# Performance work log

Hardware: AMD Instinct MI355X
Metric: run time of the kernel (lower is better)

Reference implementation:

```python
import jax, jax.numpy as jnp
import numpy as np

N = 50000   # drug nodes
R = 8       # relations (= n_classes)
E = 200000  # edges per relation
ED = 400000 # decoder edges


def _deg_norm(idx, n):
    deg = jax.ops.segment_sum(jnp.ones(idx.shape, jnp.float32), idx, num_segments=n)
    return jnp.where(deg > 0, jax.lax.rsqrt(jnp.maximum(deg, 1.0)), 0.0)


def hetero_conv(x, src, dst, W, b, n):
    # DGL HeteroGraphConv(sum) of GraphConv(norm='both') per relation, single node type.
    out = jnp.zeros((n, W.shape[2]), x.dtype)
    for r in range(W.shape[0]):
        s, d = src[r], dst[r]
        ns = _deg_norm(s, n)  # out-degree^{-1/2} (src norm)
        nd = _deg_norm(d, n)  # in-degree^{-1/2} (dst norm)
        m = (x * ns[:, None]) @ W[r]                       # [n, dout]
        agg = jax.ops.segment_sum(m[s], d, num_segments=n)  # gather+scatter [E, dout]
        out = out + agg * nd[:, None] + b[r]
    return out


def hgcn_layer(x, src, dst, Wa, ba, Wb, bb, n):
    h = hetero_conv(x, src, dst, Wa, ba, n)
    h = jax.nn.relu(h)
    return hetero_conv(h, src, dst, Wb, bb, n)


def setup_inputs() -> dict:
    key = jax.random.key(0)
    ks = jax.random.split(key, 16)
    s = 0.02
    return {
        "node2_features": jax.random.normal(ks[0], (N, 256), jnp.float32),
        "mpnn_features": jax.random.normal(ks[1], (N, 300), jnp.float32),
        "src": jax.random.randint(ks[2], (R, E), 0, N, jnp.int32),
        "dst": jax.random.randint(ks[3], (R, E), 0, N, jnp.int32),
        "dec_src": jax.random.randint(ks[4], (ED,), 0, N, jnp.int32),
        "dec_dst": jax.random.randint(ks[5], (ED,), 0, N, jnp.int32),
        "W2a": jax.random.normal(ks[6], (R, 256, 256), jnp.float32) * s,
        "b2a": jnp.zeros((R, 256), jnp.float32),
        "W2b": jax.random.normal(ks[7], (R, 256, 128), jnp.float32) * s,
        "b2b": jnp.zeros((R, 128), jnp.float32),
        "W3a": jax.random.normal(ks[8], (R, 300, 256), jnp.float32) * s,
        "b3a": jnp.zeros((R, 256), jnp.float32),
        "W3b": jax.random.normal(ks[9], (R, 256, 128), jnp.float32) * s,
        "b3b": jnp.zeros((R, 128), jnp.float32),
        "Wp1": jax.random.normal(ks[10], (512, 256), jnp.float32) * s,
        "bp1": jnp.zeros((256,), jnp.float32),
        "Wp2": jax.random.normal(ks[11], (256, R), jnp.float32) * s,
        "bp2": jnp.zeros((R,), jnp.float32),
    }


def reference(node2_features, mpnn_features, src, dst, dec_src, dec_dst,
              W2a, b2a, W2b, b2b, W3a, b3a, W3b, b3b, Wp1, bp1, Wp2, bp2):
    h2 = hgcn_layer(node2_features, src, dst, W2a, b2a, W2b, b2b, N)  # [N, 128]
    h3 = hgcn_layer(mpnn_features, src, dst, W3a, b3a, W3b, b3b, N)   # [N, 128]
    feat = jnp.concatenate([h2, h3], axis=1)                            # [N, 256]
    # edge-wise gather-concat-MLP (note: original has NO relu between W1 and W2)
    x = jnp.concatenate([feat[dec_src], feat[dec_dst]], axis=1)          # [ED, 512]
    score = (x @ Wp1 + bp1) @ Wp2 + bp2                                  # [ED, R]
    return score
```

## Files before the change

### kernel.cpp

```cpp
#include <hip/hip_runtime.h>
#include <hip/hip_bf16.h>

#define NN 50000
#define RR 8
#define EE 200000
#define EDD 400000
#define SCB 196
#define CH 5000
#define CHK 16

typedef __attribute__((ext_vector_type(8))) short short8;
typedef __attribute__((ext_vector_type(4))) float floatx4;

static __device__ __forceinline__ unsigned short f2bf(float f) {
    union { float f; unsigned u; } v; v.f = f;
    unsigned r = v.u + 0x7fff + ((v.u >> 16) & 1);
    return (unsigned short)(r >> 16);
}
static __device__ __forceinline__ float bf2f(unsigned short h) {
    union { unsigned u; float f; } v; v.u = ((unsigned)h) << 16;
    return v.f;
}
static __device__ __forceinline__ void gload_lds16(const unsigned short* g, unsigned short* l) {
    __builtin_amdgcn_global_load_lds(
        (const __attribute__((address_space(1))) void*)g,
        (__attribute__((address_space(3))) void*)l,
        16, 0, 0);
}

__global__ __launch_bounds__(256) void k_histp(const int* __restrict__ src, const int* __restrict__ dst,
                                               unsigned char* __restrict__ tmp) {
    __shared__ unsigned lh[12512];
    int chunk = blockIdx.x, r = blockIdx.y, which = blockIdx.z;
    const int* idx = (which ? dst : src) + (size_t)r * EE;
    for (int i = threadIdx.x; i < 12512; i += 256) lh[i] = 0;
    __syncthreads();
    int e0 = chunk * (EE / CHK);
    for (int e = e0 + threadIdx.x; e < e0 + EE / CHK; e += 256) {
        int n = idx[e];
        atomicAdd(&lh[n >> 2], 1u << ((n & 3) * 8));
    }
    __syncthreads();
    unsigned* t = (unsigned*)(tmp + (((size_t)(which * RR + r) * CHK + chunk) * 50048));
    for (int i = threadIdx.x; i < 12512; i += 256) t[i] = lh[i];
}

__global__ void k_reduce(const unsigned char* __restrict__ tmp,
                         int* __restrict__ outdeg, int* __restrict__ indeg) {
    int i = blockIdx.x * 256 + threadIdx.x;
    if (i >= 2 * RR * 12512) return;
    int wr = i / 12512;
    int wd = i - wr * 12512;
    unsigned s0 = 0, s1 = 0, s2 = 0, s3 = 0;
    const unsigned* base = (const unsigned*)(tmp + (size_t)wr * CHK * 50048) + wd;
    #pragma unroll
    for (int c = 0; c < CHK; c++) {
        unsigned v = base[(size_t)c * 12512];
        s0 += v & 255u; s1 += (v >> 8) & 255u; s2 += (v >> 16) & 255u; s3 += (v >> 24) & 255u;
    }
    int which = wr / RR, r = wr - which * RR;
    int n = wd * 4;
    int* deg = (which ? indeg : outdeg) + (size_t)r * NN;
    if (n < NN) {
        deg[n] = (int)s0;
        if (n + 1 < NN) deg[n + 1] = (int)s1;
        if (n + 2 < NN) deg[n + 2] = (int)s2;
        if (n + 3 < NN) deg[n + 3] = (int)s3;
    }
}

__global__ void k_norms(int* __restrict__ outdeg, int* __restrict__ indeg) {
    int i = blockIdx.x * blockDim.x + threadIdx.x;
    if (i >= RR * NN) return;
    int od = outdeg[i];
    int id = indeg[i];
    ((float*)outdeg)[i] = od > 0 ? rsqrtf((float)od) : 0.f;
    ((float*)indeg)[i]  = id > 0 ? rsqrtf((float)id) : 0.f;
}

__global__ void k_scanA(const int* __restrict__ indeg, int* __restrict__ bsum) {
    int r = blockIdx.y;
    int i = blockIdx.x * 256 + threadIdx.x;
    int v = (i < NN) ? indeg[(size_t)r * NN + i] : 0;
    #pragma unroll
    for (int d = 32; d > 0; d >>= 1) v += __shfl_down(v, d, 64);
    __shared__ int ws4[4];
    if ((threadIdx.x & 63) == 0) ws4[threadIdx.x >> 6] = v;
    __syncthreads();
    if (threadIdx.x == 0) bsum[r * SCB + blockIdx.x] = ws4[0] + ws4[1] + ws4[2] + ws4[3];
}

__global__ void k_scanB(int* __restrict__ bsum, int* __restrict__ offs) {
    int r = blockIdx.x;
    int t = threadIdx.x;
    int v = (t < SCB) ? bsum[r * SCB + t] : 0;
    int lane = t & 63, wid = t >> 6;
    int sv = v;
    #pragma unroll
    for (int d = 1; d < 64; d <<= 1) {
        int u = __shfl_up(sv, d, 64);
        if (lane >= d) sv += u;
    }
    __shared__ int wsum[4];
    if (lane == 63) wsum[wid] = sv;
    __syncthreads();
    int add = 0;
    for (int x = 0; x < wid; x++) add += wsum[x];
    int incl = sv + add;
    if (t < SCB) bsum[r * SCB + t] = incl - v;
    if (t == 255) offs[(size_t)r * (NN + 1) + NN] = incl;
}

__global__ void k_scanC(const int* __restrict__ indeg, const int* __restrict__ bsum,
                        int* __restrict__ offs) {
    int r = blockIdx.y;
    int i = blockIdx.x * 256 + threadIdx.x;
    int v = (i < NN) ? indeg[(size_t)r * NN + i] : 0;
    int lane = threadIdx.x & 63, wid = threadIdx.x >> 6;
    int sv = v;
    #pragma unroll
    for (int d = 1; d < 64; d <<= 1) {
        int u = __shfl_up(sv, d, 64);
        if (lane >= d) sv += u;
    }
    __shared__ int wsum[4];
    if (lane == 63) wsum[wid] = sv;
    __syncthreads();
    int add = bsum[r * SCB + blockIdx.x];
    for (int x = 0; x < wid; x++) add += wsum[x];
    if (i < NN) offs[(size_t)r * (NN + 1) + i] = sv - v + add;
}

__global__ void k_fillw(const int* __restrict__ src, const int* __restrict__ dst,
                        const int* __restrict__ offs, const float* __restrict__ ns,
                        int* __restrict__ cursor, int2* __restrict__ csrw) {
    int i = blockIdx.x * blockDim.x + threadIdx.x;
    if (i >= RR * EE) return;
    int r = i / EE;
    int s = src[i], d = dst[i];
    int pos = offs[r * (NN + 1) + d] + atomicAdd(&cursor[r * NN + d], 1);
    int2 v;
    v.x = s;
    v.y = __float_as_int(ns[(size_t)r * NN + s]);
    csrw[(size_t)r * EE + pos] = v;
}

__global__ void k_prep(const float* __restrict__ Wp1, const float* __restrict__ Wp2,
                       const float* __restrict__ bp1, const float* __restrict__ bp2,
                       const float* __restrict__ b2a, const float* __restrict__ b2b,
                       const float* __restrict__ b3a, const float* __restrict__ b3b,
                       float* __restrict__ Mcat, float* __restrict__ cvec,
                       float* __restrict__ bs) {
    int bx = blockIdx.x;
    if (bx < 16) {
        int t = bx * 256 + threadIdx.x;
        int i = t >> 4, j = t & 15;
        int half = j >> 3, jj = j & 7;
        const float* wrow = Wp1 + (size_t)(half * 256 + i) * 256;
        float s = 0.f;
        for (int k = 0; k < 256; k++) s += wrow[k] * Wp2[k * 8 + jj];
        Mcat[i * 16 + j] = s;
    } else if (bx == 16) {
        int j = threadIdx.x;
        if (j < 8) {
            float s = bp2[j];
            for (int k = 0; k < 256; k++) s += bp1[k] * Wp2[k * 8 + j];
            cvec[j] = s;
        }
    } else {
        int j = threadIdx.x;
        float s = 0.f;
        for (int r = 0; r < RR; r++) s += b2a[r * 256 + j];
        bs[j] = s;
        if (j < 128) {
            s = 0.f;
            for (int r = 0; r < RR; r++) s += b2b[r * 128 + j];
            bs[256 + j] = s;
        }
        s = 0.f;
        for (int r = 0; r < RR; r++) s += b3a[r * 256 + j];
        bs[512 + j] = s;
        if (j < 128) {
            s = 0.f;
            for (int r = 0; r < RR; r++) s += b3b[r * 128 + j];
            bs[768 + j] = s;
        }
    }
}

__global__ void k_fold(const float* __restrict__ W2b, const float* __restrict__ W3b,
                       const float* __restrict__ Mcat, const float* __restrict__ bs,
                       unsigned short* __restrict__ FmatT, float* __restrict__ cfold) {
    int bx = blockIdx.x;
    if (bx < 256) {
        int idx = bx * 256 + threadIdx.x;
        int rj = idx >> 9, i = idx & 511;
        int r = rj >> 4, j = rj & 15;
        float s = 0.f;
        if (i < 256) {
            const float* wr = W2b + ((size_t)r * 256 + i) * 128;
            for (int c = 0; c < 128; c++) s += wr[c] * Mcat[c * 16 + j];
        } else {
            const float* wr = W3b + ((size_t)r * 256 + (i - 256)) * 128;
            for (int c = 0; c < 128; c++) s += wr[c] * Mcat[(128 + c) * 16 + j];
        }
        FmatT[(size_t)rj * 512 + i] = f2bf(s);
    } else {
        int j = threadIdx.x;
        if (j < 16) {
            float s = 0.f;
            for (int c = 0; c < 128; c++)
                s += bs[256 + c] * Mcat[c * 16 + j] + bs[768 + c] * Mcat[(128 + c) * 16 + j];
            cfold[j] = s;
        }
    }
}

__global__ void k_castx(const float* __restrict__ x2, const float* __restrict__ x3,
                        unsigned short* __restrict__ XH) {
    int i = blockIdx.x * 256 + threadIdx.x;
    if (i >= NN * 560) return;
    int row = i / 560, col = i - row * 560;
    float v;
    if (col < 256) v = x2[(size_t)row * 256 + col];
    else if (col < 556) v = x3[(size_t)row * 300 + (col - 256)];
    else v = 0.f;
    XH[i] = f2bf(v);
}

__global__ void k_wt2(const float* __restrict__ W2a, const float* __restrict__ W3a,
                      unsigned short* __restrict__ WT2, unsigned short* __restrict__ WT3) {
    const float* W; unsigned short* WT; int K0, Kpad;
    if (blockIdx.y == 0) { W = W2a; WT = WT2; K0 = 256; Kpad = 256; }
    else                 { W = W3a; WT = WT3; K0 = 300; Kpad = 304; }
    int i = blockIdx.x * 256 + threadIdx.x;
    int total = 256 * RR * Kpad;
    if (i >= total) return;
    int n = i / (RR * Kpad);
    int rem = i - n * (RR * Kpad);
    int r = rem / Kpad;
    int k = rem - r * Kpad;
    float v = (k < K0) ? W[((size_t)r * K0 + k) * 256 + n] : 0.f;
    WT[i] = f2bf(v);
}

__global__ __launch_bounds__(256) void k_aggp(
        const unsigned short* __restrict__ xb,
        const int2* __restrict__ csrw, const int* __restrict__ offs,
        const float* __restrict__ nd, int nbase,
        unsigned short* __restrict__ Y2, unsigned short* __restrict__ Y3) {
    int lane = threadIdx.x & 63;
    int sub = threadIdx.x >> 6;
    int h = lane >> 5;
    int l = lane & 31;
    int bn = blockIdx.x * 4 + sub;
    int n = nbase + bn;
    int r = blockIdx.y;
    int o0 = offs[r * (NN + 1) + n];
    int o1 = offs[r * (NN + 1) + n + 1];
    o0 = __builtin_amdgcn_readfirstlane(o0);
    o1 = __builtin_amdgcn_readfirstlane(o1);
    int cnt = o1 - o0;
    float ndv = nd[(size_t)r * NN + n];
    const int2* cs = csrw + (size_t)r * EE + o0;
    bool tl = l < 6;
    float va[8], vb[8], vc[8];
    #pragma unroll
    for (int q = 0; q < 8; q++) { va[q] = 0.f; vb[q] = 0.f; vc[q] = 0.f; }

    for (int eb = 0; eb < cnt; eb += 64) {
        int rem = cnt - eb;
        int2 rec = cs[eb + min(lane, rem - 1)];
        int kmax = rem < 64 ? rem : 64;
        for (int kb = 0; kb < kmax; kb += 8) {
            #pragma unroll
            for (int u = 0; u < 4; u++) {
                int k = kb + 2 * u + h;
                int kk = k < kmax - 1 ? k : kmax - 1;
                int sidx = __shfl(rec.x, kk, 64);
                float f = __int_as_float(__shfl(rec.y, kk, 64));
                if (k >= kmax) f = 0.f;
                const unsigned short* p = xb + (size_t)(unsigned)sidx * 560;
                short8 A = *(const short8*)(p + l * 8);
                short8 B = *(const short8*)(p + 256 + l * 8);
                #pragma unroll
                for (int q = 0; q < 8; q++) {
                    va[q] += f * bf2f((unsigned short)A[q]);
                    vb[q] += f * bf2f((unsigned short)B[q]);
                }
                if (tl) {
                    short8 C = *(const short8*)(p + 512 + l * 8);
                    #pragma unroll
                    for (int q = 0; q < 8; q++) vc[q] += f * bf2f((unsigned short)C[q]);
                }
            }
        }
    }
    #pragma unroll
    for (int q = 0; q < 8; q++) {
        va[q] += __shfl_xor(va[q], 32, 64);
        vb[q] += __shfl_xor(vb[q], 32, 64);
        vc[q] += __shfl_xor(vc[q], 32, 64);
    }
    if (h == 0) {
        short8 o2, o3;
        #pragma unroll
        for (int q = 0; q < 8; q++) {
            o2[q] = (short)f2bf(va[q] * ndv);
            o3[q] = (short)f2bf(vb[q] * ndv);
        }
        *(short8*)(Y2 + (size_t)bn * 2048 + r * 256 + l * 8) = o2;
        *(short8*)(Y3 + (size_t)bn * 2432 + r * 304 + l * 8) = o3;
        if (tl) {
            short8 oc;
            #pragma unroll
            for (int q = 0; q < 8; q++) oc[q] = (short)f2bf(vc[q] * ndv);
            *(short8*)(Y3 + (size_t)bn * 2432 + r * 304 + 256 + l * 8) = oc;
        }
    }
}

template<int TN>
__global__ __launch_bounds__(256) void k_gemm_bf(
        const unsigned short* __restrict__ A, int lda,
        const unsigned short* __restrict__ BT, int ldb,
        const float* __restrict__ bias,
        const float* __restrict__ Cin, int ldcin,
        void* __restrict__ Cout, int ldc,
        int M, int K, int flags) {
    constexpr int BN = TN * 32;
    __shared__ unsigned short As[128 * 64];
    __shared__ unsigned short Bs[BN * 64];
    int m0 = blockIdx.x * 128;
    int n0 = blockIdx.y * BN;
    int t = threadIdx.x;
    int w = t >> 6, l = t & 63;
    int qm = (w >> 1) * 64, qn = (w & 1) * (TN * 16);
    int lr = l & 15, lg = l >> 4;
    int lrow = l >> 3;
    int lch  = (l & 7) ^ lrow;

    floatx4 acc[4][TN];
    #pragma unroll
    for (int a = 0; a < 4; a++)
        #pragma unroll
        for (int b = 0; b < TN; b++)
            acc[a][b] = (floatx4){0.f, 0.f, 0.f, 0.f};

    for (int k0 = 0; k0 < K; k0 += 64) {
        #pragma unroll
        for (int j = 0; j < 4; j++) {
            int seg = w * 4 + j;
            int gr = m0 + seg * 8 + lrow; if (gr > M - 1) gr = M - 1;
            gload_lds16(A + (size_t)gr * lda + k0 + lch * 8, &As[seg * 512]);
        }
        #pragma unroll
        for (int j = 0; j < TN; j++) {
            int seg = w * TN + j;
            int row = n0 + seg * 8 + lrow;
            gload_lds16(BT + (size_t)row * ldb + k0 + lch * 8, &Bs[seg * 512]);
        }
        __syncthreads();
        #pragma unroll
        for (int ks = 0; ks < 2; ks++) {
            int slot = ((ks * 4 + lg) ^ (lr & 7)) * 8;
            short8 af[4], bf[TN];
            #pragma unroll
            for (int i = 0; i < 4; i++)
                af[i] = *(const short8*)&As[(qm + i * 16 + lr) * 64 + slot];
            #pragma unroll
            for (int i = 0; i < TN; i++)
                bf[i] = *(const short8*)&Bs[(qn + i * 16 + lr) * 64 + slot];
            #pragma unroll
            for (int tm = 0; tm < 4; tm++)
                #pragma unroll
                for (int tn = 0; tn < TN; tn++)
                    acc[tm][tn] = __builtin_amdgcn_mfma_f32_16x16x32_bf16(
                        af[tm], bf[tn], acc[tm][tn], 0, 0, 0);
        }
        __syncthreads();
    }

    int addbias = flags & 1, accum = flags & 2, relu = flags & 4, outbf = flags & 8;
    #pragma unroll
    for (int tm = 0; tm < 4; tm++) {
        int rbase = m0 + qm + tm * 16 + lg * 4;
        #pragma unroll
        for (int reg = 0; reg < 4; reg++) {
            int row = rbase + reg;
            if (row >= M) continue;
            #pragma unroll
            for (int tn = 0; tn < TN; tn++) {
                int col = n0 + qn + tn * 16 + lr;
                float v = acc[tm][tn][reg];
                if (addbias) v += bias[col];
                if (accum) v += Cin[(size_t)row * ldcin + col];
                if (relu) v = fmaxf(v, 0.f);
                if (outbf) ((unsigned short*)Cout)[(size_t)row * ldc + col] = f2bf(v);
                else       ((float*)Cout)[(size_t)row * ldc + col] = v;
            }
        }
    }
}

__global__ __launch_bounds__(256) void k_gemm2(
        const unsigned short* __restrict__ Y2, const unsigned short* __restrict__ Y3,
        const unsigned short* __restrict__ WT2, const unsigned short* __restrict__ WT3,
        const float* __restrict__ bs, unsigned short* __restrict__ hb,
        int nbase, int M) {
    __shared__ unsigned short As[64 * 64];
    __shared__ unsigned short Bs[64 * 64];
    int z = blockIdx.z;
    const unsigned short* A  = z ? Y3 : Y2;
    const unsigned short* BT = z ? WT3 : WT2;
    int lda = z ? 2432 : 2048;
    int K = lda;
    const float* bias = bs + z * 512;
    int m0 = blockIdx.x * 64;
    int n0 = blockIdx.y * 64;
    int t = threadIdx.x;
    int w = t >> 6, l = t & 63;
    int qm = (w >> 1) * 32, qn = (w & 1) * 32;
    int lr = l & 15, lg = l >> 4;
    int lrow = l >> 3;
    int lch  = (l & 7) ^ lrow;

    floatx4 acc[2][2];
    #pragma unroll
    for (int a = 0; a < 2; a++)
        #pragma unroll
        for (int b = 0; b < 2; b++)
            acc[a][b] = (floatx4){0.f, 0.f, 0.f, 0.f};

    for (int k0 = 0; k0 < K; k0 += 64) {
        #pragma unroll
        for (int j = 0; j < 2; j++) {
            int seg = w * 2 + j;
            int gr = m0 + seg * 8 + lrow; if (gr > M - 1) gr = M - 1;
            gload_lds16(A + (size_t)gr * lda + k0 + lch * 8, &As[seg * 512]);
        }
        #pragma unroll
        for (int j = 0; j < 2; j++) {
            int seg = w * 2 + j;
            int row = n0 + seg * 8 + lrow;
            gload_lds16(BT + (size_t)row * lda + k0 + lch * 8, &Bs[seg * 512]);
        }
        __syncthreads();
        #pragma unroll
        for (int ks = 0; ks < 2; ks++) {
            int slot = ((ks * 4 + lg) ^ (lr & 7)) * 8;
            short8 af[2], bf[2];
            #pragma unroll
            for (int i = 0; i < 2; i++)
                af[i] = *(const short8*)&As[(qm + i * 16 + lr) * 64 + slot];
            #pragma unroll
            for (int i = 0; i < 2; i++)
                bf[i] = *(const short8*)&Bs[(qn + i * 16 + lr) * 64 + slot];
            #pragma unroll
            for (int tm = 0; tm < 2; tm++)
                #pragma unroll
                for (int tn = 0; tn < 2; tn++)
                    acc[tm][tn] = __builtin_amdgcn_mfma_f32_16x16x32_bf16(
                        af[tm], bf[tn], acc[tm][tn], 0, 0, 0);
        }
        __syncthreads();
    }

    #pragma unroll
    for (int tm = 0; tm < 2; tm++) {
        int rbase = m0 + qm + tm * 16 + lg * 4;
        #pragma unroll
        for (int reg = 0; reg < 4; reg++) {
            int row = rbase + reg;
            if (row >= M) continue;
            #pragma unroll
            for (int tn = 0; tn < 2; tn++) {
                int col = n0 + qn + tn * 16 + lr;
                float v = fmaxf(acc[tm][tn][reg] + bias[col], 0.f);
                hb[(size_t)(nbase + row) * 512 + z * 256 + col] = f2bf(v);
            }
        }
    }
}

__global__ __launch_bounds__(256) void k_aggAB(
        const int2* __restrict__ csrw, const int* __restrict__ offs,
        const float* __restrict__ nd, const float* __restrict__ G,
        const float* __restrict__ cfold, const float* __restrict__ cvec,
        float* __restrict__ AB) {
    int lane = threadIdx.x & 63, sub = threadIdx.x >> 6;
    int n = blockIdx.x * 4 + sub;
    int slot = lane >> 4, j = lane & 15;
    int jb = slot << 4;
    float acc = 0.f;
    for (int hh = 0; hh < 2; hh++) {
        int r = slot + hh * 4;
        int o0 = offs[r * (NN + 1) + n];
        int o1 = offs[r * (NN + 1) + n + 1];
        float ndv = nd[(size_t)r * NN + n];
        const int2* cs = csrw + (size_t)r * EE + o0;
        int cnt = o1 - o0;
        float t0 = 0.f, t1 = 0.f;
        for (int eb = 0; eb < cnt; eb += 16) {
            int rem = cnt - eb;
            int2 rec = cs[eb + min(j, rem - 1)];
            int kmax = rem < 16 ? rem : 16;
            for (int k = 0; k < kmax; k += 2) {
                int s0 = __shfl(rec.x, jb + k, 64);
                float f0 = __int_as_float(__shfl(rec.y, jb + k, 64));
                int k1 = k + 1 < kmax ? k + 1 : kmax - 1;
                int s1 = __shfl(rec.x, jb + k1, 64);
                float f1 = (k + 1 < kmax) ? __int_as_float(__shfl(rec.y, jb + k1, 64)) : 0.f;
                t0 += f0 * G[(size_t)(unsigned)s0 * 128 + r * 16 + j];
                t1 += f1 * G[(size_t)(unsigned)s1 * 128 + r * 16 + j];
            }
        }
        acc += ndv * (t0 + t1);
    }
    acc += __shfl_xor(acc, 16, 64);
    acc += __shfl_xor(acc, 32, 64);
    if (lane < 16) AB[(size_t)n * 16 + j] = acc + cfold[j] + (j < 8 ? cvec[j] : 0.f);
}

__global__ void k_dec(const int* __restrict__ dsrc, const int* __restrict__ ddst,
                      const float* __restrict__ AB, float* __restrict__ out) {
    int e = blockIdx.x * 256 + threadIdx.x;
    if (e >= EDD) return;
    int s = dsrc[e], d = ddst[e];
    const float4* as = (const float4*)(AB + (size_t)s * 16);
    const float4* ad = (const float4*)(AB + (size_t)d * 16 + 8);
    float4 x0 = as[0], x1 = as[1], y0 = ad[0], y1 = ad[1];
    float4 o0 = {x0.x + y0.x, x0.y + y0.y, x0.z + y0.z, x0.w + y0.w};
    float4 o1 = {x1.x + y1.x, x1.y + y1.y, x1.z + y1.z, x1.w + y1.w};
    float4* op = (float4*)(out + (size_t)e * 8);
    op[0] = o0; op[1] = o1;
}

extern "C" void kernel_launch(void* const* d_in, const int* in_sizes, int n_in,
                              void* d_out, int out_size, void* d_ws, size_t ws_size,
                              hipStream_t stream) {
    const float* x2  = (const float*)d_in[0];
    const float* x3  = (const float*)d_in[1];
    const int*   src = (const int*)d_in[2];
    const int*   dst = (const int*)d_in[3];
    const int*   dsrc = (const int*)d_in[4];
    const int*   ddst = (const int*)d_in[5];
    const float* W2a = (const float*)d_in[6];
    const float* b2a = (const float*)d_in[7];
    const float* W2b = (const float*)d_in[8];
    const float* b2b = (const float*)d_in[9];
    const float* W3a = (const float*)d_in[10];
    const float* b3a = (const float*)d_in[11];
    const float* W3b = (const float*)d_in[12];
    const float* b3b = (const float*)d_in[13];
    const float* Wp1 = (const float*)d_in[14];
    const float* bp1 = (const float*)d_in[15];
    const float* Wp2 = (const float*)d_in[16];
    const float* bp2 = (const float*)d_in[17];
    float* out = (float*)d_out;

    char* ws = (char*)d_ws;
    size_t off = 0;
    auto alloc = [&](size_t nbytes) {
        char* p = ws + off;
        off += nbytes;
        off = (off + 255) & ~(size_t)255;
        return p;
    };
    float* ns   = (float*)alloc((size_t)RR * NN * 4);
    float* nd   = (float*)alloc((size_t)RR * NN * 4);
    int*   offs = (int*)alloc((size_t)RR * (NN + 1) * 4);
    int2*  csrw = (int2*)alloc((size_t)RR * EE * 8);
    unsigned short* XH     = (unsigned short*)alloc((size_t)NN * 560 * 2);
    unsigned short* hbuf23 = (unsigned short*)alloc((size_t)NN * 512 * 2);
    unsigned short* WT2a   = (unsigned short*)alloc((size_t)256 * 2048 * 2);
    unsigned short* WT3a   = (unsigned short*)alloc((size_t)256 * 2432 * 2);
    unsigned short* FmatT  = (unsigned short*)alloc((size_t)128 * 512 * 2);
    char* YR = alloc((size_t)CH * (2048 + 2432) * 2);
    float* Mcat  = (float*)alloc(4096 * 4);
    float* cvec  = (float*)alloc(64 * 4);
    float* bsums = (float*)alloc(1024 * 4);
    float* cfold = (float*)alloc(64 * 4);
    int*   bsum  = (int*)alloc((size_t)RR * SCB * 4);

    unsigned short* Y2a = (unsigned short*)YR;
    unsigned short* Y3a = Y2a + (size_t)CH * 2048;
    int*   outdeg = (int*)ns;
    int*   indeg  = (int*)nd;
    int*   cursor = (int*)YR;
    unsigned char* htmp = (unsigned char*)(YR + (4 << 20));
    float* G      = (float*)YR;
    float* AB     = (float*)(YR + (size_t)NN * 128 * 4);

    hipMemsetAsync(cursor, 0, (size_t)RR * NN * 4, stream);

    k_histp<<<dim3(CHK, RR, 2), 256, 0, stream>>>(src, dst, htmp);
    k_reduce<<<(2 * RR * 12512 + 255) / 256, 256, 0, stream>>>(htmp, outdeg, indeg);
    k_scanA<<<dim3(SCB, RR), 256, 0, stream>>>(indeg, bsum);
    k_scanB<<<RR, 256, 0, stream>>>(bsum, offs);
    k_scanC<<<dim3(SCB, RR), 256, 0, stream>>>(indeg, bsum, offs);
    k_norms<<<(RR * NN + 255) / 256, 256, 0, stream>>>(outdeg, indeg);
    int edgeBlocks = (RR * EE + 255) / 256;
    k_fillw<<<edgeBlocks, 256, 0, stream>>>(src, dst, offs, ns, cursor, csrw);
    k_prep<<<18, 256, 0, stream>>>(Wp1, Wp2, bp1, bp2, b2a, b2b, b3a, b3b, Mcat, cvec, bsums);
    k_fold<<<257, 256, 0, stream>>>(W2b, W3b, Mcat, bsums, FmatT, cfold);

    k_castx<<<(NN * 560 + 255) / 256, 256, 0, stream>>>(x2, x3, XH);
    k_wt2<<<dim3((256 * RR * 304 + 255) / 256, 2), 256, 0, stream>>>(W2a, W3a, WT2a, WT3a);

    for (int c = 0; c < NN / CH; c++) {
        k_aggp<<<dim3(CH / 4, RR), 256, 0, stream>>>(XH, csrw, offs, nd, c * CH, Y2a, Y3a);
        k_gemm2<<<dim3((CH + 63) / 64, 4, 2), 256, 0, stream>>>(
            Y2a, Y3a, WT2a, WT3a, bsums, hbuf23, c * CH, CH);
    }

    k_gemm_bf<1><<<dim3((NN + 127) / 128, 4), 256, 0, stream>>>(
        hbuf23, 512, FmatT, 512, bsums, (const float*)nullptr, 0,
        (void*)G, 128, NN, 512, 0);

    k_aggAB<<<NN / 4, 256, 0, stream>>>(csrw, offs, nd, G, cfold, cvec, AB);
    k_dec<<<(EDD + 255) / 256, 256, 0, stream>>>(dsrc, ddst, AB, out);
}
```

Measured before the change: 1.158 ms.

## Build CSR with shared-memory cursors per node range and widen aggregation lanes

Replaces the global-atomic CSR fill, and the memset of its cursor array, with a kernel where each block owns a range of destination nodes per relation. The block scans all edges of its relation, keeps cursors in LDS and places only the edges that land in its range. The aggregation kernel now has each lane handle 8 contiguous bf16 features, so one wave reads a full 512-element row per edge. This replaces the half-wave split and the cross-half reduction. Each fill block reads every edge of its relation and only 64 blocks are launched, which limits parallelism, and the aggregation loop now handles one edge per step instead of two.

```diff
diff --git a/kernel.cpp b/kernel.cpp
--- a/kernel.cpp
+++ b/kernel.cpp
@@ -8,6 +8,8 @@
 #define SCB 196
 #define CH 5000
 #define CHK 16
+#define FR 8
+#define FRN 6250
 
 typedef __attribute__((ext_vector_type(8))) short short8;
 typedef __attribute__((ext_vector_type(4))) float floatx4;
@@ -131,18 +133,35 @@
     if (i < NN) offs[(size_t)r * (NN + 1) + i] = sv - v + add;
 }
 
-__global__ void k_fillw(const int* __restrict__ src, const int* __restrict__ dst,
-                        const int* __restrict__ offs, const float* __restrict__ ns,
-                        int* __restrict__ cursor, int2* __restrict__ csrw) {
-    int i = blockIdx.x * blockDim.x + threadIdx.x;
-    if (i >= RR * EE) return;
-    int r = i / EE;
-    int s = src[i], d = dst[i];
-    int pos = offs[r * (NN + 1) + d] + atomicAdd(&cursor[r * NN + d], 1);
-    int2 v;
-    v.x = s;
-    v.y = __float_as_int(ns[(size_t)r * NN + s]);
-    csrw[(size_t)r * EE + pos] = v;
+__global__ __launch_bounds__(256) void k_fillw2(const int* __restrict__ src, const int* __restrict__ dst,
+                                                const int* __restrict__ offs, const float* __restrict__ ns,
+                                                int2* __restrict__ csrw) {
+    __shared__ int cur[FRN];
+    int range = blockIdx.x, r = blockIdx.y;
+    int lo = range * FRN;
+    for (int i = threadIdx.x; i < FRN; i += 256) cur[i] = 0;
+    __syncthreads();
+    const int4* sp = (const int4*)(src + (size_t)r * EE);
+    const int4* dp = (const int4*)(dst + (size_t)r * EE);
+    const int* offr = offs + r * (NN + 1);
+    const float* nsr = ns + (size_t)r * NN;
+    int2* cw = csrw + (size_t)r * EE;
+    for (int e4 = threadIdx.x; e4 < EE / 4; e4 += 256) {
+        int4 d4 = dp[e4];
+        int4 s4 = sp[e4];
+        #pragma unroll
+        for (int u = 0; u < 4; u++) {
+            int d = (u == 0 ? d4.x : u == 1 ? d4.y : u == 2 ? d4.z : d4.w) - lo;
+            if ((unsigned)d < (unsigned)FRN) {
+                int s = (u == 0 ? s4.x : u == 1 ? s4.y : u == 2 ? s4.z : s4.w);
+                int pos = offr[lo + d] + atomicAdd(&cur[d], 1);
+                int2 v;
+                v.x = s;
+                v.y = __float_as_int(nsr[s]);
+                cw[pos] = v;
+            }
+        }
+    }
 }
 
 __global__ void k_prep(const float* __restrict__ Wp1, const float* __restrict__ Wp2,
@@ -251,8 +270,6 @@
         unsigned short* __restrict__ Y2, unsigned short* __restrict__ Y3) {
     int lane = threadIdx.x & 63;
     int sub = threadIdx.x >> 6;
-    int h = lane >> 5;
-    int l = lane & 31;
     int bn = blockIdx.x * 4 + sub;
     int n = nbase + bn;
     int r = blockIdx.y;
@@ -263,60 +280,47 @@
     int cnt = o1 - o0;
     float ndv = nd[(size_t)r * NN + n];
     const int2* cs = csrw + (size_t)r * EE + o0;
-    bool tl = l < 6;
-    float va[8], vb[8], vc[8];
-    #pragma unroll
-    for (int q = 0; q < 8; q++) { va[q] = 0.f; vb[q] = 0.f; vc[q] = 0.f; }
+    bool tl = lane < 6;
+    float va[8], vc[8];
+    #pragma unroll
+    for (int q = 0; q < 8; q++) { va[q] = 0.f; vc[q] = 0.f; }
 
     for (int eb = 0; eb < cnt; eb += 64) {
         int rem = cnt - eb;
         int2 rec = cs[eb + min(lane, rem - 1)];
         int kmax = rem < 64 ? rem : 64;
-        for (int kb = 0; kb < kmax; kb += 8) {
+        for (int kb = 0; kb < kmax; kb += 4) {
             #pragma unroll
             for (int u = 0; u < 4; u++) {
-                int k = kb + 2 * u + h;
-                int kk = k < kmax - 1 ? k : kmax - 1;
-                int sidx = __shfl(rec.x, kk, 64);
-                float f = __int_as_float(__shfl(rec.y, kk, 64));
-                if (k >= kmax) f = 0.f;
+                int k = kb + u;
+                if (k >= kmax) break;
+                int sidx = __shfl(rec.x, k, 64);
+                float f = __int_as_float(__shfl(rec.y, k, 64));
                 const unsigned short* p = xb + (size_t)(unsigned)sidx * 560;
-                short8 A = *(const short8*)(p + l * 8);
-                short8 B = *(const short8*)(p + 256 + l * 8);
+                short8 M = *(const short8*)(p + lane * 8);
                 #pragma unroll
-                for (int q = 0; q < 8; q++) {
-                    va[q] += f * bf2f((unsigned short)A[q]);
-                    vb[q] += f * bf2f((unsigned short)B[q]);
-                }
+                for (int q = 0; q < 8; q++) va[q] += f * bf2f((unsigned short)M[q]);
                 if (tl) {
-                    short8 C = *(const short8*)(p + 512 + l * 8);
+                    short8 C = *(const short8*)(p + 512 + lane * 8);
                     #pragma unroll
                     for (int q = 0; q < 8; q++) vc[q] += f * bf2f((unsigned short)C[q]);
                 }
             }
         }
     }
-    #pragma unroll
-    for (int q = 0; q < 8; q++) {
-        va[q] += __shfl_xor(va[q], 32, 64);
-        vb[q] += __shfl_xor(vb[q], 32, 64);
-        vc[q] += __shfl_xor(vc[q], 32, 64);
-    }
-    if (h == 0) {
-        short8 o2, o3;
-        #pragma unroll
-        for (int q = 0; q < 8; q++) {
-            o2[q] = (short)f2bf(va[q] * ndv);
-            o3[q] = (short)f2bf(vb[q] * ndv);
-        }
-        *(short8*)(Y2 + (size_t)bn * 2048 + r * 256 + l * 8) = o2;
-        *(short8*)(Y3 + (size_t)bn * 2432 + r * 304 + l * 8) = o3;
-        if (tl) {
-            short8 oc;
-            #pragma unroll
-            for (int q = 0; q < 8; q++) oc[q] = (short)f2bf(vc[q] * ndv);
-            *(short8*)(Y3 + (size_t)bn * 2432 + r * 304 + 256 + l * 8) = oc;
-        }
+    short8 o;
+    #pragma unroll
+    for (int q = 0; q < 8; q++) o[q] = (short)f2bf(va[q] * ndv);
+    if (lane < 32) {
+        *(short8*)(Y2 + (size_t)bn * 2048 + r * 256 + lane * 8) = o;
+    } else {
+        *(short8*)(Y3 + (size_t)bn * 2432 + r * 304 + (lane - 32) * 8) = o;
+    }
+    if (tl) {
+        short8 oc;
+        #pragma unroll
+        for (int q = 0; q < 8; q++) oc[q] = (short)f2bf(vc[q] * ndv);
+        *(short8*)(Y3 + (size_t)bn * 2432 + r * 304 + 256 + lane * 8) = oc;
     }
 }
 
@@ -587,12 +591,9 @@
     unsigned short* Y3a = Y2a + (size_t)CH * 2048;
     int*   outdeg = (int*)ns;
     int*   indeg  = (int*)nd;
-    int*   cursor = (int*)YR;
-    unsigned char* htmp = (unsigned char*)(YR + (4 << 20));
+    unsigned char* htmp = (unsigned char*)YR;
     float* G      = (float*)YR;
     float* AB     = (float*)(YR + (size_t)NN * 128 * 4);
-
-    hipMemsetAsync(cursor, 0, (size_t)RR * NN * 4, stream);
 
     k_histp<<<dim3(CHK, RR, 2), 256, 0, stream>>>(src, dst, htmp);
     k_reduce<<<(2 * RR * 12512 + 255) / 256, 256, 0, stream>>>(htmp, outdeg, indeg);
@@ -600,8 +601,7 @@
     k_scanB<<<RR, 256, 0, stream>>>(bsum, offs);
     k_scanC<<<dim3(SCB, RR), 256, 0, stream>>>(indeg, bsum, offs);
     k_norms<<<(RR * NN + 255) / 256, 256, 0, stream>>>(outdeg, indeg);
-    int edgeBlocks = (RR * EE + 255) / 256;
-    k_fillw<<<edgeBlocks, 256, 0, stream>>>(src, dst, offs, ns, cursor, csrw);
+    k_fillw2<<<dim3(FR, RR), 256, 0, stream>>>(src, dst, offs, ns, csrw);
     k_prep<<<18, 256, 0, stream>>>(Wp1, Wp2, bp1, bp2, b2a, b2b, b3a, b3b, Mcat, cvec, bsums);
     k_fold<<<257, 256, 0, stream>>>(W2b, W3b, Mcat, bsums, FmatT, cfold);
 
```

Measured after the change: 1.419 ms. 22.6% more time.
